# Performance work log

Measured on AMD Instinct MI355X. Metric: run time of the kernel, lower is better.

Reference implementation:

```python
import jax, jax.numpy as jnp
import numpy as np

N_HEAD = 16
DIMS = 1024

def setup_inputs() -> dict:
    key = jax.random.key(0)
    ks = jax.random.split(key, 5)
    B, T, C = 4, 2048, DIMS
    std = 1.0 / np.sqrt(C)
    x = jax.random.normal(ks[0], (B, T, C), dtype=jnp.float32)
    W_attn = jax.random.normal(ks[1], (C, 3 * C), dtype=jnp.float32) * std
    b_attn = jnp.zeros((3 * C,), dtype=jnp.float32)
    W_proj = jax.random.normal(ks[2], (C, C), dtype=jnp.float32) * std
    b_proj = jnp.zeros((C,), dtype=jnp.float32)
    return {"x": x, "W_attn": W_attn, "b_attn": b_attn, "W_proj": W_proj, "b_proj": b_proj}

def reference(x, W_attn, b_attn, W_proj, b_proj):
    B, T, C = x.shape
    H = N_HEAD
    D = C // H
    qkv = x @ W_attn + b_attn  # [B,T,3C]
    q, k, v = jnp.split(qkv, 3, axis=-1)
    # [B,T,C] -> [B,H,T,D]
    q = q.reshape(B, T, H, D).transpose(0, 2, 1, 3)
    k = k.reshape(B, T, H, D).transpose(0, 2, 1, 3)
    v = v.reshape(B, T, H, D).transpose(0, 2, 1, 3)
    att = jnp.einsum('bhqd,bhkd->bhqk', q, k) * (1.0 / np.sqrt(D))
    causal = jnp.tril(jnp.ones((T, T), dtype=bool))  # [T,T]
    att = jnp.where(causal[None, None, :, :], att, -jnp.inf)
    att = jax.nn.softmax(att, axis=-1)
    # dropout p=0.0 -> identity in eval/zero-prob mode
    y = jnp.einsum('bhqk,bhkd->bhqd', att, v)  # [B,H,T,D]
    y = y.transpose(0, 2, 1, 3).reshape(B, T, C)
    y = y @ W_proj + b_proj
    return y
```

## Files before the change

kernel.cpp:

```cpp
#include <hip/hip_runtime.h>
#include <hip/hip_bf16.h>
#include <stdint.h>

typedef unsigned short u16;
typedef unsigned int   u32;

using short8 = __attribute__((ext_vector_type(8))) short;
using f32x4  = __attribute__((ext_vector_type(4))) float;

__device__ __forceinline__ float b2f(u32 u) {
    union { u32 i; float f; } v;
    v.i = u << 16;
    return v.f;
}
__device__ __forceinline__ u16 f2b(float f) {
    union { float f; u32 i; } v; v.f = f;
    u32 x = v.i;
    x += 0x7fffu + ((x >> 16) & 1u);
    return (u16)(x >> 16);
}
__device__ __forceinline__ u32 pkbf16(float lo, float hi) {
    __hip_bfloat162 h = __float22bfloat162_rn(float2{lo, hi});
    return *reinterpret_cast<u32*>(&h);
}
__device__ __forceinline__ float fexp2(float x) {
#if __has_builtin(__builtin_amdgcn_exp2f)
    return __builtin_amdgcn_exp2f(x);
#else
    return exp2f(x);
#endif
}
__device__ __forceinline__ u32 perm_lo(u32 a, u32 b) {
#if __has_builtin(__builtin_amdgcn_perm)
    return __builtin_amdgcn_perm(b, a, 0x05040100u);
#else
    return (a & 0xffffu) | (b << 16);
#endif
}
__device__ __forceinline__ u32 perm_hi(u32 a, u32 b) {
#if __has_builtin(__builtin_amdgcn_perm)
    return __builtin_amdgcn_perm(b, a, 0x07060302u);
#else
    return (a >> 16) | (b & 0xffff0000u);
#endif
}

__device__ __forceinline__ void gll16(const u16* g, u16* l) {
    __builtin_amdgcn_global_load_lds(
        (const __attribute__((address_space(1))) void*)g,
        (__attribute__((address_space(3))) void*)l, 16, 0, 0);
}

__global__ __launch_bounds__(256)
void cast_bf16(const float* __restrict__ in, u16* __restrict__ out, int n)
{
    const int i = (blockIdx.x * 256 + threadIdx.x) * 8;
    if (i >= n) return;
    const float4 a = *reinterpret_cast<const float4*>(in + i);
    const float4 b = *reinterpret_cast<const float4*>(in + i + 4);
    *reinterpret_cast<uint4*>(out + i) = make_uint4(
        pkbf16(a.x, a.y), pkbf16(a.z, a.w), pkbf16(b.x, b.y), pkbf16(b.z, b.w));
}

__global__ __launch_bounds__(256)
void transpose_cast2(const float* __restrict__ Wa, u16* __restrict__ Wta,
                     const float* __restrict__ Wp, u16* __restrict__ Wtp)
{
    __shared__ float t[32][33];
    constexpr int R = 1024;
    const bool pa = blockIdx.x < 96;
    const float* W  = pa ? Wa  : Wp;
    u16*         Wt = pa ? Wta : Wtp;
    const int Ncols = pa ? 3072 : 1024;
    const int c0 = (pa ? blockIdx.x : blockIdx.x - 96) * 32;
    const int r0 = blockIdx.y * 32;
    const int lx = threadIdx.x & 31, ly = threadIdx.x >> 5;
#pragma unroll
    for (int i = 0; i < 4; i++) {
        const int r = ly + i * 8;
        t[r][lx] = W[(size_t)(r0 + r) * Ncols + c0 + lx];
    }
    __syncthreads();
#pragma unroll
    for (int i = 0; i < 4; i++) {
        const int c = ly + i * 8;
        Wt[(size_t)(c0 + c) * R + r0 + lx] = f2b(t[lx][c]);
    }
}

template<typename OT>
__global__ __launch_bounds__(256)
void gemm_mfma(const u16* __restrict__ A, const u16* __restrict__ Bt,
               const float* __restrict__ bias, OT* __restrict__ C,
               int M, int N, int K)
{
    __shared__ u16 As[128 * 32];
    __shared__ u16 Bs[128 * 32];

    const int tid  = threadIdx.x;
    const int w    = tid >> 6;
    const int lane = tid & 63;
    const int quad = lane >> 4;
    const int c16  = lane & 15;
    const int wr   = w >> 1, wc = w & 1;

    const int m0 = blockIdx.y * 128;
    const int n0 = blockIdx.x * 128;

    const int srow = w * 32 + (lane >> 2);
    const int skc  = (lane & 3) * 8;
    const u16* gA = A  + (size_t)(m0 + srow) * K + skc;
    const u16* gB = Bt + (size_t)(n0 + srow) * K + skc;
    u16* lA = As + w * 32 * 32 + lane * 8;
    u16* lB = Bs + w * 32 * 32 + lane * 8;

    f32x4 acc[4][4];
#pragma unroll
    for (int i = 0; i < 4; i++)
#pragma unroll
        for (int j = 0; j < 4; j++) acc[i][j] = (f32x4){0.f, 0.f, 0.f, 0.f};

    for (int k0 = 0; k0 < K; k0 += 32) {
        __syncthreads();
        gll16(gA + k0,                  lA);
        gll16(gA + k0 + 16 * (size_t)K, lA + 16 * 32);
        gll16(gB + k0,                  lB);
        gll16(gB + k0 + 16 * (size_t)K, lB + 16 * 32);
        __syncthreads();

        short8 af[4], bf[4];
#pragma unroll
        for (int i = 0; i < 4; i++)
            af[i] = *reinterpret_cast<const short8*>(&As[(wr * 64 + i * 16 + c16) * 32 + quad * 8]);
#pragma unroll
        for (int j = 0; j < 4; j++)
            bf[j] = *reinterpret_cast<const short8*>(&Bs[(wc * 64 + j * 16 + c16) * 32 + quad * 8]);
#pragma unroll
        for (int i = 0; i < 4; i++)
#pragma unroll
            for (int j = 0; j < 4; j++)
                acc[i][j] = __builtin_amdgcn_mfma_f32_16x16x32_bf16(af[i], bf[j], acc[i][j], 0, 0, 0);
    }

#pragma unroll
    for (int i = 0; i < 4; i++)
#pragma unroll
        for (int j = 0; j < 4; j++) {
            const int colg = n0 + wc * 64 + j * 16 + c16;
            const float bv = bias[colg];
#pragma unroll
            for (int r = 0; r < 4; r++) {
                const int rowg = m0 + wr * 64 + i * 16 + quad * 4 + r;
                const float v = acc[i][j][r] + bv;
                if constexpr (sizeof(OT) == 2)
                    ((u16*)C)[(size_t)rowg * N + colg] = f2b(v);
                else
                    ((float*)C)[(size_t)rowg * N + colg] = v;
            }
        }
}

__global__ __launch_bounds__(512, 2)
void gemm_mfma_256(const u16* __restrict__ A, const u16* __restrict__ Bt,
                   const float* __restrict__ bias, u16* __restrict__ C,
                   int M, int N, int K)
{
    __shared__ u16 ring[4 * 16384];

    const int tid  = threadIdx.x;
    const int w    = tid >> 6;
    const int lane = tid & 63;
    const int quad = lane >> 4;
    const int c16  = lane & 15;
    const int wr   = w >> 2;
    const int wc   = w & 3;

    const int nwg  = gridDim.x * gridDim.y;
    const int orig = blockIdx.y * gridDim.x + blockIdx.x;
    const int swz  = (orig & 7) * (nwg >> 3) + (orig >> 3);
    const int bx   = swz % gridDim.x;
    const int by   = swz / gridDim.x;
    const int m0   = by * 256, n0 = bx * 256;

    const int r0s = w * 16 + (lane >> 2);
    const int qs  = (lane & 3) ^ ((r0s >> 1) & 3);
    const u16* gA = A  + (size_t)(m0 + r0s) * K + qs * 8;
    const u16* gB = Bt + (size_t)(n0 + r0s) * K + qs * 8;
    const size_t hstep = (size_t)128 * K;
    u16* dstB = ring + w * 512 + lane * 8;

    const int slot = quad ^ ((c16 >> 1) & 3);
    const int aoff = (wr * 128 + c16) * 32 + slot * 8;
    const int boff = 8192 + (wc * 64 + c16) * 32 + slot * 8;

    f32x4 acc[8][4];
#pragma unroll
    for (int i = 0; i < 8; i++)
#pragma unroll
        for (int j = 0; j < 4; j++) acc[i][j] = (f32x4){0.f, 0.f, 0.f, 0.f};

    const int nt = K >> 5;

#pragma unroll
    for (int t = 0; t < 3; t++) {
        u16* db = dstB + t * 16384;
        const size_t ko = (size_t)t * 32;
        gll16(gA + ko,         db);
        gll16(gA + ko + hstep, db + 4096);
        gll16(gB + ko,         db + 8192);
        gll16(gB + ko + hstep, db + 12288);
    }

#pragma unroll 1
    for (int t = 0; t < nt; t++) {
        const int remain = nt - 1 - t;
        if (remain >= 2)      asm volatile("s_waitcnt vmcnt(8)" ::: "memory");
        else if (remain == 1) asm volatile("s_waitcnt vmcnt(4)" ::: "memory");
        else                  asm volatile("s_waitcnt vmcnt(0)" ::: "memory");
        asm volatile("s_barrier" ::: "memory");

        const u16* buf = ring + (t & 3) * 16384;
        const bool pf  = (t + 3) < nt;
        u16* db = dstB + ((t + 3) & 3) * 16384;
        const size_t ko = (size_t)(t + 3) * 32;

        short8 bfr[4], afr[4];

#pragma unroll
        for (int j = 0; j < 4; j++)
            bfr[j] = *reinterpret_cast<const short8*>(buf + boff + j * 512);
#pragma unroll
        for (int i = 0; i < 4; i++)
            afr[i] = *reinterpret_cast<const short8*>(buf + aoff + i * 512);
        if (pf) { gll16(gA + ko, db); gll16(gA + ko + hstep, db + 4096); }
        asm volatile("s_waitcnt lgkmcnt(0)" ::: "memory");
        __builtin_amdgcn_sched_barrier(0);
        __builtin_amdgcn_s_setprio(1);
#pragma unroll
        for (int i = 0; i < 4; i++)
#pragma unroll
            for (int j = 0; j < 4; j++)
                acc[i][j] = __builtin_amdgcn_mfma_f32_16x16x32_bf16(afr[i], bfr[j], acc[i][j], 0, 0, 0);
        __builtin_amdgcn_s_setprio(0);
        asm volatile("s_barrier" ::: "memory");

#pragma unroll
        for (int i = 0; i < 4; i++)
            afr[i] = *reinterpret_cast<const short8*>(buf + aoff + (i + 4) * 512);
        if (pf) { gll16(gB + ko, db + 8192); gll16(gB + ko + hstep, db + 12288); }
        asm volatile("s_waitcnt lgkmcnt(0)" ::: "memory");
        __builtin_amdgcn_sched_barrier(0);
        __builtin_amdgcn_s_setprio(1);
#pragma unroll
        for (int i = 0; i < 4; i++)
#pragma unroll
            for (int j = 0; j < 4; j++)
                acc[i + 4][j] = __builtin_amdgcn_mfma_f32_16x16x32_bf16(afr[i], bfr[j], acc[i + 4][j], 0, 0, 0);
        __builtin_amdgcn_s_setprio(0);
        asm volatile("s_barrier" ::: "memory");
    }

    float bv[4];
#pragma unroll
    for (int j = 0; j < 4; j++) bv[j] = bias[n0 + wc * 64 + j * 16 + c16];

    const int erow = wr * 16 + quad * 4;
    const int ecol = wc * 64 + c16;
#pragma unroll
    for (int i = 0; i < 8; i++) {
#pragma unroll
        for (int j = 0; j < 4; j++)
#pragma unroll
            for (int r = 0; r < 4; r++)
                ring[(erow + r) * 264 + ecol + j * 16] = f2b(acc[i][j][r] + bv[j]);
        __syncthreads();
#pragma unroll
        for (int rr = 0; rr < 2; rr++) {
            const int lr = rr * 16 + (tid >> 5);
            const int cc = (tid & 31) * 8;
            const uint4 vvec = *reinterpret_cast<const uint4*>(&ring[lr * 264 + cc]);
            const int gr = m0 + (lr >> 4) * 128 + i * 16 + (lr & 15);
            *reinterpret_cast<uint4*>(&C[(size_t)gr * N + n0 + cc]) = vvec;
        }
        __syncthreads();
    }
}

struct TileState {
    f32x4 O[4];
    float m, l;
    short8 qf[2];
    int qglob;
};

__device__ __forceinline__ void tile_pass(
    const u16* __restrict__ Ks, const u16* __restrict__ Vt,
    u16* __restrict__ plrow,
    TileState& ts, int kt0, bool diag, int quad, int c16)
{
    const int x7 = c16 & 7;

    f32x4 s[4];
    __builtin_amdgcn_s_setprio(1);
#pragma unroll
    for (int sub = 0; sub < 4; sub++) {
        const int row = sub * 16 + c16;
        short8 kf0 = *reinterpret_cast<const short8*>(&Ks[row * 64 + ((0 + quad) ^ x7) * 8]);
        short8 kf1 = *reinterpret_cast<const short8*>(&Ks[row * 64 + ((4 + quad) ^ x7) * 8]);
        f32x4 acc = (f32x4){0.f, 0.f, 0.f, 0.f};
        acc = __builtin_amdgcn_mfma_f32_16x16x32_bf16(kf0, ts.qf[0], acc, 0, 0, 0);
        acc = __builtin_amdgcn_mfma_f32_16x16x32_bf16(kf1, ts.qf[1], acc, 0, 0, 0);
        s[sub] = acc;
    }
    __builtin_amdgcn_s_setprio(0);

    if (diag) {
#pragma unroll
        for (int sub = 0; sub < 4; sub++)
#pragma unroll
            for (int r = 0; r < 4; r++)
                if (kt0 + sub * 16 + quad * 4 + r > ts.qglob) s[sub][r] = -INFINITY;
    }

    float m0a = fmaxf(fmaxf(s[0][0], s[0][1]), fmaxf(s[0][2], s[0][3]));
    float m1a = fmaxf(fmaxf(s[1][0], s[1][1]), fmaxf(s[1][2], s[1][3]));
    float m2a = fmaxf(fmaxf(s[2][0], s[2][1]), fmaxf(s[2][2], s[2][3]));
    float m3a = fmaxf(fmaxf(s[3][0], s[3][1]), fmaxf(s[3][2], s[3][3]));
    float mloc = fmaxf(fmaxf(m0a, m1a), fmaxf(m2a, m3a));
    mloc = fmaxf(mloc, __shfl_xor(mloc, 16));
    mloc = fmaxf(mloc, __shfl_xor(mloc, 32));

    if (!__all(mloc <= ts.m + 8.f)) {
        const float mnew = fmaxf(ts.m, mloc);
        const float al   = fexp2(ts.m - mnew);
        ts.m = mnew;
        ts.l *= al;
#pragma unroll
        for (int r = 0; r < 4; r++) {
            const float alr = __shfl(al, quad * 4 + r);
#pragma unroll
            for (int d = 0; d < 4; d++) ts.O[d][r] *= alr;
        }
    }

    float ls = 0.f;
#pragma unroll
    for (int sub = 0; sub < 4; sub++) {
#pragma unroll
        for (int r = 0; r < 4; r++) s[sub][r] = fexp2(s[sub][r] - ts.m);
        ls += (s[sub][0] + s[sub][1]) + (s[sub][2] + s[sub][3]);
        *reinterpret_cast<uint2*>(
            plrow + c16 * 64 + ((sub * 2 + (quad >> 1)) ^ x7) * 8 + (quad & 1) * 4) =
            make_uint2(pkbf16(s[sub][0], s[sub][1]), pkbf16(s[sub][2], s[sub][3]));
    }
    ts.l += ls;

    short8 pf[2];
#pragma unroll
    for (int c = 0; c < 2; c++)
        pf[c] = *reinterpret_cast<const short8*>(
            plrow + c16 * 64 + ((c * 4 + quad) ^ x7) * 8);

    __builtin_amdgcn_s_setprio(1);
#pragma unroll
    for (int dsub = 0; dsub < 4; dsub++) {
        const int row = dsub * 16 + c16;
#pragma unroll
        for (int c = 0; c < 2; c++) {
            short8 vf = *reinterpret_cast<const short8*>(&Vt[row * 64 + ((c * 4 + quad) ^ x7) * 8]);
            ts.O[dsub] = __builtin_amdgcn_mfma_f32_16x16x32_bf16(pf[c], vf, ts.O[dsub], 0, 0, 0);
        }
    }
    __builtin_amdgcn_s_setprio(0);
}

__global__ __launch_bounds__(256)
void attn_flash(const u16* __restrict__ qkv, u16* __restrict__ out)
{
    constexpr int T = 2048, C = 1024, C3 = 3072;

    __shared__ u16 Ks[2][64 * 64];
    __shared__ u16 Vt[2][64 * 64];
    __shared__ u16 Pl[4][16 * 64];

    const int tid  = threadIdx.x;
    const int w    = tid >> 6;
    const int lane = tid & 63;
    const int quad = lane >> 4;
    const int c16  = lane & 15;

    const int flat = blockIdx.y * gridDim.x + blockIdx.x;
    const int xcd  = flat & 7;
    const int tt   = flat >> 3;
    const int qp   = tt & 15;
    const int bh   = ((tt >> 4) << 3) | xcd;
    const int qtA  = qp;
    const int qtB  = 31 - qp;
    const int h    = bh & 15;
    const int b    = bh >> 4;

    const int kr  = tid >> 2, kq = tid & 3;
    const int vkp = tid & 31, vdg = (tid >> 5) * 8;
    const u16* baseK = qkv + (size_t)(b * T + kr) * C3 + C + h * 64 + kq * 16;
    const u16* baseV = qkv + (size_t)(b * T + 2 * vkp) * C3 + 2 * C + h * 64 + vdg;

    const int kx  = kr & 7;
    const int kd0 = kr * 64 + ((2 * kq + 0) ^ kx) * 8;
    const int kd1 = kr * 64 + ((2 * kq + 1) ^ kx) * 8;
    const int vslot = vkp >> 2, vintra = (vkp & 3) * 2;

    u16* plrow = &Pl[w][0];

    uint4 ka, kb, va, vb;

#pragma unroll 1
    for (int phase = 0; phase < 2; ++phase) {
        const int qt = phase ? qtA : qtB;

        TileState ts;
        ts.qglob = qt * 64 + w * 16 + c16;
        ts.m = -INFINITY;
        ts.l = 0.f;
#pragma unroll
        for (int d = 0; d < 4; d++) ts.O[d] = (f32x4){0.f, 0.f, 0.f, 0.f};
        constexpr float QSCALE = 0.125f * 1.44269504089f;
#pragma unroll
        for (int c = 0; c < 2; c++) {
            short8 rq = *reinterpret_cast<const short8*>(
                qkv + (size_t)(b * T + ts.qglob) * C3 + h * 64 + c * 32 + quad * 8);
#pragma unroll
            for (int j = 0; j < 8; j++)
                ts.qf[c][j] = (short)f2b(b2f((u16)rq[j]) * QSCALE);
        }

        {
            const uint4* gp = reinterpret_cast<const uint4*>(baseK);
            ka = gp[0]; kb = gp[1];
            va = *reinterpret_cast<const uint4*>(baseV);
            vb = *reinterpret_cast<const uint4*>(baseV + C3);
        }
        __syncthreads();
        {
            *reinterpret_cast<uint4*>(&Ks[0][kd0]) = ka;
            *reinterpret_cast<uint4*>(&Ks[0][kd1]) = kb;
            const u32* aw = reinterpret_cast<const u32*>(&va);
            const u32* bw = reinterpret_cast<const u32*>(&vb);
#pragma unroll
            for (int i = 0; i < 4; i++) {
                const int d0 = vdg + 2 * i;
                *reinterpret_cast<u32*>(&Vt[0][d0 * 64 + (vslot ^ (2 * i)) * 8 + vintra]) =
                    perm_lo(aw[i], bw[i]);
                *reinterpret_cast<u32*>(&Vt[0][(d0 + 1) * 64 + (vslot ^ (2 * i + 1)) * 8 + vintra]) =
                    perm_hi(aw[i], bw[i]);
            }
        }

        for (int kt = 0; kt <= qt; kt++) {
            const int cur = kt & 1;
            __syncthreads();

            if (kt < qt) {
                const int nk0 = (kt + 1) * 64;
                const uint4* gp = reinterpret_cast<const uint4*>(baseK + (size_t)nk0 * C3);
                ka = gp[0]; kb = gp[1];
                const u16* g0 = baseV + (size_t)nk0 * C3;
                va = *reinterpret_cast<const uint4*>(g0);
                vb = *reinterpret_cast<const uint4*>(g0 + C3);
            }

            tile_pass(Ks[cur], Vt[cur], plrow, ts, kt * 64, kt == qt, quad, c16);

            if (kt < qt) {
                const int nxt = cur ^ 1;
                *reinterpret_cast<uint4*>(&Ks[nxt][kd0]) = ka;
                *reinterpret_cast<uint4*>(&Ks[nxt][kd1]) = kb;
                const u32* aw = reinterpret_cast<const u32*>(&va);
                const u32* bw = reinterpret_cast<const u32*>(&vb);
#pragma unroll
                for (int i = 0; i < 4; i++) {
                    const int d0 = vdg + 2 * i;
                    *reinterpret_cast<u32*>(&Vt[nxt][d0 * 64 + (vslot ^ (2 * i)) * 8 + vintra]) =
                        perm_lo(aw[i], bw[i]);
                    *reinterpret_cast<u32*>(&Vt[nxt][(d0 + 1) * 64 + (vslot ^ (2 * i + 1)) * 8 + vintra]) =
                        perm_hi(aw[i], bw[i]);
                }
            }
        }

        float ls = ts.l;
        ls += __shfl_xor(ls, 16);
        ls += __shfl_xor(ls, 32);
        const float inv = 1.0f / ls;
#pragma unroll
        for (int r = 0; r < 4; r++) {
            const float invr = __shfl(inv, quad * 4 + r);
            const int qrow = qt * 64 + w * 16 + quad * 4 + r;
#pragma unroll
            for (int dsub = 0; dsub < 4; dsub++)
                out[(size_t)(b * T + qrow) * C + h * 64 + dsub * 16 + c16] =
                    f2b(ts.O[dsub][r] * invr);
        }
    }
}

extern "C" void kernel_launch(void* const* d_in, const int* in_sizes, int n_in,
                              void* d_out, int out_size, void* d_ws, size_t ws_size,
                              hipStream_t stream)
{
    constexpr int B = 4, T = 2048, C = 1024;
    constexpr int M = B * T;
    const float* x      = (const float*)d_in[0];
    const float* W_attn = (const float*)d_in[1];
    const float* b_attn = (const float*)d_in[2];
    const float* W_proj = (const float*)d_in[3];
    const float* b_proj = (const float*)d_in[4];
    float* out = (float*)d_out;

    char* p = (char*)d_ws;
    u16* qkv     = (u16*)p;                 p += (size_t)M * 3 * C * sizeof(u16);
    u16* xb      = (u16*)p;
    u16* attn_o  = (u16*)p;                 p += (size_t)M * C * sizeof(u16);
    u16* Wt_attn = (u16*)p;                 p += (size_t)3 * C * C * sizeof(u16);
    u16* Wt_proj = (u16*)p;

    cast_bf16<<<dim3(M * C / (256 * 8)), 256, 0, stream>>>(x, xb, M * C);
    transpose_cast2<<<dim3(128, 32), 256, 0, stream>>>(W_attn, Wt_attn, W_proj, Wt_proj);

    gemm_mfma_256<<<dim3(3 * C / 256, M / 256), 512, 0, stream>>>(
        xb, Wt_attn, b_attn, qkv, M, 3 * C, C);

    attn_flash<<<dim3(16, B * 16), 256, 0, stream>>>(qkv, attn_o);

    gemm_mfma<float><<<dim3(C / 128, M / 128), 256, 0, stream>>>(
        attn_o, Wt_proj, b_proj, out, M, C, C);
}
```

Baseline: 270.4 us.

## Process 128-row query tiles per block with two 16-row groups per wave

Each wave now handles 32 query rows as two independent 16-row groups that share every K and V fragment loaded from LDS, so the block covers a 128-row query tile. The grid is halved to 8x64 blocks, each still pairing a low and a high query tile for causal load balance. The aim is to halve the number of K/V tile loads per query row and raise the ratio of MFMA work to LDS traffic. The cost is doubled accumulator and softmax state per wave, with higher register pressure, fewer blocks in flight, and some wasted work on partially masked diagonal tiles.

```diff
diff --git a/kernel.cpp b/kernel.cpp
--- a/kernel.cpp
+++ b/kernel.cpp
@@ -286,80 +286,88 @@
     }
 }
 
-struct TileState {
-    f32x4 O[4];
-    float m, l;
-    short8 qf[2];
-    int qglob;
+struct TileState2 {
+    f32x4 O[2][4];
+    float m[2], l[2];
+    short8 qf[2][2];
+    int qbase;
 };
 
-__device__ __forceinline__ void tile_pass(
+__device__ __forceinline__ void tile_pass2(
     const u16* __restrict__ Ks, const u16* __restrict__ Vt,
     u16* __restrict__ plrow,
-    TileState& ts, int kt0, bool diag, int quad, int c16)
+    TileState2& ts, int kt0, int quad, int c16)
 {
     const int x7 = c16 & 7;
 
-    f32x4 s[4];
+    f32x4 s[2][4];
     __builtin_amdgcn_s_setprio(1);
 #pragma unroll
     for (int sub = 0; sub < 4; sub++) {
         const int row = sub * 16 + c16;
         short8 kf0 = *reinterpret_cast<const short8*>(&Ks[row * 64 + ((0 + quad) ^ x7) * 8]);
         short8 kf1 = *reinterpret_cast<const short8*>(&Ks[row * 64 + ((4 + quad) ^ x7) * 8]);
-        f32x4 acc = (f32x4){0.f, 0.f, 0.f, 0.f};
-        acc = __builtin_amdgcn_mfma_f32_16x16x32_bf16(kf0, ts.qf[0], acc, 0, 0, 0);
-        acc = __builtin_amdgcn_mfma_f32_16x16x32_bf16(kf1, ts.qf[1], acc, 0, 0, 0);
-        s[sub] = acc;
+        f32x4 a0 = (f32x4){0.f, 0.f, 0.f, 0.f};
+        a0 = __builtin_amdgcn_mfma_f32_16x16x32_bf16(kf0, ts.qf[0][0], a0, 0, 0, 0);
+        s[0][sub] = __builtin_amdgcn_mfma_f32_16x16x32_bf16(kf1, ts.qf[0][1], a0, 0, 0, 0);
+        f32x4 a1 = (f32x4){0.f, 0.f, 0.f, 0.f};
+        a1 = __builtin_amdgcn_mfma_f32_16x16x32_bf16(kf0, ts.qf[1][0], a1, 0, 0, 0);
+        s[1][sub] = __builtin_amdgcn_mfma_f32_16x16x32_bf16(kf1, ts.qf[1][1], a1, 0, 0, 0);
     }
     __builtin_amdgcn_s_setprio(0);
 
-    if (diag) {
-#pragma unroll
-        for (int sub = 0; sub < 4; sub++)
-#pragma unroll
-            for (int r = 0; r < 4; r++)
-                if (kt0 + sub * 16 + quad * 4 + r > ts.qglob) s[sub][r] = -INFINITY;
-    }
-
-    float m0a = fmaxf(fmaxf(s[0][0], s[0][1]), fmaxf(s[0][2], s[0][3]));
-    float m1a = fmaxf(fmaxf(s[1][0], s[1][1]), fmaxf(s[1][2], s[1][3]));
-    float m2a = fmaxf(fmaxf(s[2][0], s[2][1]), fmaxf(s[2][2], s[2][3]));
-    float m3a = fmaxf(fmaxf(s[3][0], s[3][1]), fmaxf(s[3][2], s[3][3]));
-    float mloc = fmaxf(fmaxf(m0a, m1a), fmaxf(m2a, m3a));
-    mloc = fmaxf(mloc, __shfl_xor(mloc, 16));
-    mloc = fmaxf(mloc, __shfl_xor(mloc, 32));
-
-    if (!__all(mloc <= ts.m + 8.f)) {
-        const float mnew = fmaxf(ts.m, mloc);
-        const float al   = fexp2(ts.m - mnew);
-        ts.m = mnew;
-        ts.l *= al;
-#pragma unroll
-        for (int r = 0; r < 4; r++) {
-            const float alr = __shfl(al, quad * 4 + r);
-#pragma unroll
-            for (int d = 0; d < 4; d++) ts.O[d][r] *= alr;
-        }
-    }
-
-    float ls = 0.f;
-#pragma unroll
-    for (int sub = 0; sub < 4; sub++) {
-#pragma unroll
-        for (int r = 0; r < 4; r++) s[sub][r] = fexp2(s[sub][r] - ts.m);
-        ls += (s[sub][0] + s[sub][1]) + (s[sub][2] + s[sub][3]);
-        *reinterpret_cast<uint2*>(
-            plrow + c16 * 64 + ((sub * 2 + (quad >> 1)) ^ x7) * 8 + (quad & 1) * 4) =
-            make_uint2(pkbf16(s[sub][0], s[sub][1]), pkbf16(s[sub][2], s[sub][3]));
-    }
-    ts.l += ls;
-
-    short8 pf[2];
-#pragma unroll
-    for (int c = 0; c < 2; c++)
-        pf[c] = *reinterpret_cast<const short8*>(
-            plrow + c16 * 64 + ((c * 4 + quad) ^ x7) * 8);
+#pragma unroll
+    for (int g = 0; g < 2; g++) {
+        const int qg = ts.qbase + g * 16 + c16;
+        if (kt0 + 63 > ts.qbase + g * 16) {
+#pragma unroll
+            for (int sub = 0; sub < 4; sub++)
+#pragma unroll
+                for (int r = 0; r < 4; r++)
+                    if (kt0 + sub * 16 + quad * 4 + r > qg) s[g][sub][r] = -INFINITY;
+        }
+
+        float m0a = fmaxf(fmaxf(s[g][0][0], s[g][0][1]), fmaxf(s[g][0][2], s[g][0][3]));
+        float m1a = fmaxf(fmaxf(s[g][1][0], s[g][1][1]), fmaxf(s[g][1][2], s[g][1][3]));
+        float m2a = fmaxf(fmaxf(s[g][2][0], s[g][2][1]), fmaxf(s[g][2][2], s[g][2][3]));
+        float m3a = fmaxf(fmaxf(s[g][3][0], s[g][3][1]), fmaxf(s[g][3][2], s[g][3][3]));
+        float mloc = fmaxf(fmaxf(m0a, m1a), fmaxf(m2a, m3a));
+        mloc = fmaxf(mloc, __shfl_xor(mloc, 16));
+        mloc = fmaxf(mloc, __shfl_xor(mloc, 32));
+
+        if (!__all(mloc <= ts.m[g] + 8.f)) {
+            const float mnew = fmaxf(ts.m[g], mloc);
+            const float al   = fexp2(ts.m[g] - mnew);
+            ts.m[g] = mnew;
+            ts.l[g] *= al;
+#pragma unroll
+            for (int r = 0; r < 4; r++) {
+                const float alr = __shfl(al, quad * 4 + r);
+#pragma unroll
+                for (int d = 0; d < 4; d++) ts.O[g][d][r] *= alr;
+            }
+        }
+
+        float ls = 0.f;
+#pragma unroll
+        for (int sub = 0; sub < 4; sub++) {
+#pragma unroll
+            for (int r = 0; r < 4; r++) s[g][sub][r] = fexp2(s[g][sub][r] - ts.m[g]);
+            ls += (s[g][sub][0] + s[g][sub][1]) + (s[g][sub][2] + s[g][sub][3]);
+            *reinterpret_cast<uint2*>(
+                plrow + (g * 16 + c16) * 64 + ((sub * 2 + (quad >> 1)) ^ x7) * 8 + (quad & 1) * 4) =
+                make_uint2(pkbf16(s[g][sub][0], s[g][sub][1]), pkbf16(s[g][sub][2], s[g][sub][3]));
+        }
+        ts.l[g] += ls;
+    }
+
+    short8 pf[2][2];
+#pragma unroll
+    for (int g = 0; g < 2; g++)
+#pragma unroll
+        for (int c = 0; c < 2; c++)
+            pf[g][c] = *reinterpret_cast<const short8*>(
+                plrow + (g * 16 + c16) * 64 + ((c * 4 + quad) ^ x7) * 8);
 
     __builtin_amdgcn_s_setprio(1);
 #pragma unroll
@@ -368,7 +376,8 @@
 #pragma unroll
         for (int c = 0; c < 2; c++) {
             short8 vf = *reinterpret_cast<const short8*>(&Vt[row * 64 + ((c * 4 + quad) ^ x7) * 8]);
-            ts.O[dsub] = __builtin_amdgcn_mfma_f32_16x16x32_bf16(pf[c], vf, ts.O[dsub], 0, 0, 0);
+            ts.O[0][dsub] = __builtin_amdgcn_mfma_f32_16x16x32_bf16(pf[0][c], vf, ts.O[0][dsub], 0, 0, 0);
+            ts.O[1][dsub] = __builtin_amdgcn_mfma_f32_16x16x32_bf16(pf[1][c], vf, ts.O[1][dsub], 0, 0, 0);
         }
     }
     __builtin_amdgcn_s_setprio(0);
@@ -381,7 +390,7 @@
 
     __shared__ u16 Ks[2][64 * 64];
     __shared__ u16 Vt[2][64 * 64];
-    __shared__ u16 Pl[4][16 * 64];
+    __shared__ u16 Pl[4][32 * 64];
 
     const int tid  = threadIdx.x;
     const int w    = tid >> 6;
@@ -392,10 +401,10 @@
     const int flat = blockIdx.y * gridDim.x + blockIdx.x;
     const int xcd  = flat & 7;
     const int tt   = flat >> 3;
-    const int qp   = tt & 15;
-    const int bh   = ((tt >> 4) << 3) | xcd;
+    const int qp   = tt & 7;
+    const int bh   = ((tt >> 3) << 3) | xcd;
     const int qtA  = qp;
-    const int qtB  = 31 - qp;
+    const int qtB  = 15 - qp;
     const int h    = bh & 15;
     const int b    = bh >> 4;
 
@@ -417,21 +426,28 @@
     for (int phase = 0; phase < 2; ++phase) {
         const int qt = phase ? qtA : qtB;
 
-        TileState ts;
-        ts.qglob = qt * 64 + w * 16 + c16;
-        ts.m = -INFINITY;
-        ts.l = 0.f;
-#pragma unroll
-        for (int d = 0; d < 4; d++) ts.O[d] = (f32x4){0.f, 0.f, 0.f, 0.f};
+        TileState2 ts;
+        ts.qbase = qt * 128 + w * 32;
+        ts.m[0] = ts.m[1] = -INFINITY;
+        ts.l[0] = ts.l[1] = 0.f;
+#pragma unroll
+        for (int g = 0; g < 2; g++)
+#pragma unroll
+            for (int d = 0; d < 4; d++) ts.O[g][d] = (f32x4){0.f, 0.f, 0.f, 0.f};
         constexpr float QSCALE = 0.125f * 1.44269504089f;
 #pragma unroll
-        for (int c = 0; c < 2; c++) {
-            short8 rq = *reinterpret_cast<const short8*>(
-                qkv + (size_t)(b * T + ts.qglob) * C3 + h * 64 + c * 32 + quad * 8);
-#pragma unroll
-            for (int j = 0; j < 8; j++)
-                ts.qf[c][j] = (short)f2b(b2f((u16)rq[j]) * QSCALE);
-        }
+        for (int g = 0; g < 2; g++)
+#pragma unroll
+            for (int c = 0; c < 2; c++) {
+                short8 rq = *reinterpret_cast<const short8*>(
+                    qkv + (size_t)(b * T + ts.qbase + g * 16 + c16) * C3 + h * 64 + c * 32 + quad * 8);
+#pragma unroll
+                for (int j = 0; j < 8; j++)
+                    ts.qf[g][c][j] = (short)f2b(b2f((u16)rq[j]) * QSCALE);
+            }
+
+        const int ktmax = 2 * qt + 1;
+        const int qwmax = ts.qbase + 31;
 
         {
             const uint4* gp = reinterpret_cast<const uint4*>(baseK);
@@ -455,11 +471,11 @@
             }
         }
 
-        for (int kt = 0; kt <= qt; kt++) {
+        for (int kt = 0; kt <= ktmax; kt++) {
             const int cur = kt & 1;
             __syncthreads();
 
-            if (kt < qt) {
+            if (kt < ktmax) {
                 const int nk0 = (kt + 1) * 64;
                 const uint4* gp = reinterpret_cast<const uint4*>(baseK + (size_t)nk0 * C3);
                 ka = gp[0]; kb = gp[1];
@@ -468,9 +484,10 @@
                 vb = *reinterpret_cast<const uint4*>(g0 + C3);
             }
 
-            tile_pass(Ks[cur], Vt[cur], plrow, ts, kt * 64, kt == qt, quad, c16);
-
-            if (kt < qt) {
+            if (kt * 64 <= qwmax)
+                tile_pass2(Ks[cur], Vt[cur], plrow, ts, kt * 64, quad, c16);
+
+            if (kt < ktmax) {
                 const int nxt = cur ^ 1;
                 *reinterpret_cast<uint4*>(&Ks[nxt][kd0]) = ka;
                 *reinterpret_cast<uint4*>(&Ks[nxt][kd1]) = kb;
@@ -487,18 +504,21 @@
             }
         }
 
-        float ls = ts.l;
-        ls += __shfl_xor(ls, 16);
-        ls += __shfl_xor(ls, 32);
-        const float inv = 1.0f / ls;
-#pragma unroll
-        for (int r = 0; r < 4; r++) {
-            const float invr = __shfl(inv, quad * 4 + r);
-            const int qrow = qt * 64 + w * 16 + quad * 4 + r;
-#pragma unroll
-            for (int dsub = 0; dsub < 4; dsub++)
-                out[(size_t)(b * T + qrow) * C + h * 64 + dsub * 16 + c16] =
-                    f2b(ts.O[dsub][r] * invr);
+#pragma unroll
+        for (int g = 0; g < 2; g++) {
+            float ls = ts.l[g];
+            ls += __shfl_xor(ls, 16);
+            ls += __shfl_xor(ls, 32);
+            const float inv = 1.0f / ls;
+#pragma unroll
+            for (int r = 0; r < 4; r++) {
+                const float invr = __shfl(inv, quad * 4 + r);
+                const int qrow = ts.qbase + g * 16 + quad * 4 + r;
+#pragma unroll
+                for (int dsub = 0; dsub < 4; dsub++)
+                    out[(size_t)(b * T + qrow) * C + h * 64 + dsub * 16 + c16] =
+                        f2b(ts.O[g][dsub][r] * invr);
+            }
         }
     }
 }
@@ -529,7 +549,7 @@
     gemm_mfma_256<<<dim3(3 * C / 256, M / 256), 512, 0, stream>>>(
         xb, Wt_attn, b_attn, qkv, M, 3 * C, C);
 
-    attn_flash<<<dim3(16, B * 16), 256, 0, stream>>>(qkv, attn_o);
+    attn_flash<<<dim3(8, B * 16), 256, 0, stream>>>(qkv, attn_o);
 
     gemm_mfma<float><<<dim3(C / 128, M / 128), 256, 0, stream>>>(
         attn_o, Wt_proj, b_proj, out, M, C, C);
```

After: 264.7 us. -2.1%, faster.

## Use 128-row query tiles with 8 waves in flash attention; fuse prep kernels

Applied to the files above, without the earlier changes.

The attention kernel now runs 512 threads (8 waves) per block, so each block covers 128 query rows per phase instead of 64 and every K/V tile loaded into LDS is shared by twice as many waves. K and V staging is split between two halves of the block, and waves skip key tiles beyond their causal range. The grid is halved and the causal pairing of query tiles is adjusted to match. The x cast and weight transpose-cast are merged into one prep launch to save a kernel launch. Larger blocks can reduce occupancy and leave some waves idle on the diagonal tiles.

```diff
diff --git a/kernel.cpp b/kernel.cpp
--- a/kernel.cpp
+++ b/kernel.cpp
@@ -52,28 +52,29 @@
 }
 
 __global__ __launch_bounds__(256)
-void cast_bf16(const float* __restrict__ in, u16* __restrict__ out, int n)
-{
-    const int i = (blockIdx.x * 256 + threadIdx.x) * 8;
-    if (i >= n) return;
-    const float4 a = *reinterpret_cast<const float4*>(in + i);
-    const float4 b = *reinterpret_cast<const float4*>(in + i + 4);
-    *reinterpret_cast<uint4*>(out + i) = make_uint4(
-        pkbf16(a.x, a.y), pkbf16(a.z, a.w), pkbf16(b.x, b.y), pkbf16(b.z, b.w));
-}
-
-__global__ __launch_bounds__(256)
-void transpose_cast2(const float* __restrict__ Wa, u16* __restrict__ Wta,
-                     const float* __restrict__ Wp, u16* __restrict__ Wtp)
+void prep(const float* __restrict__ x, u16* __restrict__ xb,
+          const float* __restrict__ Wa, u16* __restrict__ Wta,
+          const float* __restrict__ Wp, u16* __restrict__ Wtp)
 {
     __shared__ float t[32][33];
+    const int bx = blockIdx.x;
+    if (bx < 4096) {
+        const int i = (bx * 256 + threadIdx.x) * 8;
+        const float4 a = *reinterpret_cast<const float4*>(x + i);
+        const float4 b = *reinterpret_cast<const float4*>(x + i + 4);
+        *reinterpret_cast<uint4*>(xb + i) = make_uint4(
+            pkbf16(a.x, a.y), pkbf16(a.z, a.w), pkbf16(b.x, b.y), pkbf16(b.z, b.w));
+        return;
+    }
     constexpr int R = 1024;
-    const bool pa = blockIdx.x < 96;
+    const int tb = bx - 4096;
+    const int cb = tb & 127;
+    const int r0 = (tb >> 7) * 32;
+    const bool pa = cb < 96;
     const float* W  = pa ? Wa  : Wp;
     u16*         Wt = pa ? Wta : Wtp;
     const int Ncols = pa ? 3072 : 1024;
-    const int c0 = (pa ? blockIdx.x : blockIdx.x - 96) * 32;
-    const int r0 = blockIdx.y * 32;
+    const int c0 = (pa ? cb : cb - 96) * 32;
     const int lx = threadIdx.x & 31, ly = threadIdx.x >> 5;
 #pragma unroll
     for (int i = 0; i < 4; i++) {
@@ -286,17 +287,17 @@
     }
 }
 
-struct TileState {
+struct TileState1 {
     f32x4 O[4];
     float m, l;
     short8 qf[2];
-    int qglob;
+    int qbase;
 };
 
-__device__ __forceinline__ void tile_pass(
+__device__ __forceinline__ void tile_pass1(
     const u16* __restrict__ Ks, const u16* __restrict__ Vt,
     u16* __restrict__ plrow,
-    TileState& ts, int kt0, bool diag, int quad, int c16)
+    TileState1& ts, int kt0, int quad, int c16)
 {
     const int x7 = c16 & 7;
 
@@ -307,19 +308,19 @@
         const int row = sub * 16 + c16;
         short8 kf0 = *reinterpret_cast<const short8*>(&Ks[row * 64 + ((0 + quad) ^ x7) * 8]);
         short8 kf1 = *reinterpret_cast<const short8*>(&Ks[row * 64 + ((4 + quad) ^ x7) * 8]);
-        f32x4 acc = (f32x4){0.f, 0.f, 0.f, 0.f};
-        acc = __builtin_amdgcn_mfma_f32_16x16x32_bf16(kf0, ts.qf[0], acc, 0, 0, 0);
-        acc = __builtin_amdgcn_mfma_f32_16x16x32_bf16(kf1, ts.qf[1], acc, 0, 0, 0);
-        s[sub] = acc;
+        f32x4 a = (f32x4){0.f, 0.f, 0.f, 0.f};
+        a = __builtin_amdgcn_mfma_f32_16x16x32_bf16(kf0, ts.qf[0], a, 0, 0, 0);
+        s[sub] = __builtin_amdgcn_mfma_f32_16x16x32_bf16(kf1, ts.qf[1], a, 0, 0, 0);
     }
     __builtin_amdgcn_s_setprio(0);
 
-    if (diag) {
+    if (kt0 + 63 > ts.qbase) {
+        const int qg = ts.qbase + c16;
 #pragma unroll
         for (int sub = 0; sub < 4; sub++)
 #pragma unroll
             for (int r = 0; r < 4; r++)
-                if (kt0 + sub * 16 + quad * 4 + r > ts.qglob) s[sub][r] = -INFINITY;
+                if (kt0 + sub * 16 + quad * 4 + r > qg) s[sub][r] = -INFINITY;
     }
 
     float m0a = fmaxf(fmaxf(s[0][0], s[0][1]), fmaxf(s[0][2], s[0][3]));
@@ -374,14 +375,14 @@
     __builtin_amdgcn_s_setprio(0);
 }
 
-__global__ __launch_bounds__(256)
+__global__ __launch_bounds__(512)
 void attn_flash(const u16* __restrict__ qkv, u16* __restrict__ out)
 {
     constexpr int T = 2048, C = 1024, C3 = 3072;
 
     __shared__ u16 Ks[2][64 * 64];
     __shared__ u16 Vt[2][64 * 64];
-    __shared__ u16 Pl[4][16 * 64];
+    __shared__ u16 Pl[8][16 * 64];
 
     const int tid  = threadIdx.x;
     const int w    = tid >> 6;
@@ -392,15 +393,17 @@
     const int flat = blockIdx.y * gridDim.x + blockIdx.x;
     const int xcd  = flat & 7;
     const int tt   = flat >> 3;
-    const int qp   = tt & 15;
-    const int bh   = ((tt >> 4) << 3) | xcd;
+    const int qp   = tt & 7;
+    const int bh   = ((tt >> 3) << 3) | xcd;
     const int qtA  = qp;
-    const int qtB  = 31 - qp;
+    const int qtB  = 15 - qp;
     const int h    = bh & 15;
     const int b    = bh >> 4;
 
-    const int kr  = tid >> 2, kq = tid & 3;
-    const int vkp = tid & 31, vdg = (tid >> 5) * 8;
+    const bool stK = tid < 256;
+    const int st   = stK ? tid : tid - 256;
+    const int kr  = st >> 2, kq = st & 3;
+    const int vkp = st & 31, vdg = (st >> 5) * 8;
     const u16* baseK = qkv + (size_t)(b * T + kr) * C3 + C + h * 64 + kq * 16;
     const u16* baseV = qkv + (size_t)(b * T + 2 * vkp) * C3 + 2 * C + h * 64 + vdg;
 
@@ -411,14 +414,14 @@
 
     u16* plrow = &Pl[w][0];
 
-    uint4 ka, kb, va, vb;
+    uint4 ra, rb;
 
 #pragma unroll 1
     for (int phase = 0; phase < 2; ++phase) {
         const int qt = phase ? qtA : qtB;
 
-        TileState ts;
-        ts.qglob = qt * 64 + w * 16 + c16;
+        TileState1 ts;
+        ts.qbase = qt * 128 + w * 16;
         ts.m = -INFINITY;
         ts.l = 0.f;
 #pragma unroll
@@ -427,24 +430,29 @@
 #pragma unroll
         for (int c = 0; c < 2; c++) {
             short8 rq = *reinterpret_cast<const short8*>(
-                qkv + (size_t)(b * T + ts.qglob) * C3 + h * 64 + c * 32 + quad * 8);
+                qkv + (size_t)(b * T + ts.qbase + c16) * C3 + h * 64 + c * 32 + quad * 8);
 #pragma unroll
             for (int j = 0; j < 8; j++)
                 ts.qf[c][j] = (short)f2b(b2f((u16)rq[j]) * QSCALE);
         }
 
-        {
+        const int ktmax = 2 * qt + 1;
+        const int qwmax = ts.qbase + 15;
+
+        if (stK) {
             const uint4* gp = reinterpret_cast<const uint4*>(baseK);
-            ka = gp[0]; kb = gp[1];
-            va = *reinterpret_cast<const uint4*>(baseV);
-            vb = *reinterpret_cast<const uint4*>(baseV + C3);
+            ra = gp[0]; rb = gp[1];
+        } else {
+            ra = *reinterpret_cast<const uint4*>(baseV);
+            rb = *reinterpret_cast<const uint4*>(baseV + C3);
         }
         __syncthreads();
-        {
-            *reinterpret_cast<uint4*>(&Ks[0][kd0]) = ka;
-            *reinterpret_cast<uint4*>(&Ks[0][kd1]) = kb;
-            const u32* aw = reinterpret_cast<const u32*>(&va);
-            const u32* bw = reinterpret_cast<const u32*>(&vb);
+        if (stK) {
+            *reinterpret_cast<uint4*>(&Ks[0][kd0]) = ra;
+            *reinterpret_cast<uint4*>(&Ks[0][kd1]) = rb;
+        } else {
+            const u32* aw = reinterpret_cast<const u32*>(&ra);
+            const u32* bw = reinterpret_cast<const u32*>(&rb);
 #pragma unroll
             for (int i = 0; i < 4; i++) {
                 const int d0 = vdg + 2 * i;
@@ -455,50 +463,59 @@
             }
         }
 
-        for (int kt = 0; kt <= qt; kt++) {
+        for (int kt = 0; kt <= ktmax; kt++) {
             const int cur = kt & 1;
             __syncthreads();
 
-            if (kt < qt) {
-                const int nk0 = (kt + 1) * 64;
-                const uint4* gp = reinterpret_cast<const uint4*>(baseK + (size_t)nk0 * C3);
-                ka = gp[0]; kb = gp[1];
-                const u16* g0 = baseV + (size_t)nk0 * C3;
-                va = *reinterpret_cast<const uint4*>(g0);
-                vb = *reinterpret_cast<const uint4*>(g0 + C3);
-            }
-
-            tile_pass(Ks[cur], Vt[cur], plrow, ts, kt * 64, kt == qt, quad, c16);
-
-            if (kt < qt) {
-                const int nxt = cur ^ 1;
-                *reinterpret_cast<uint4*>(&Ks[nxt][kd0]) = ka;
-                *reinterpret_cast<uint4*>(&Ks[nxt][kd1]) = kb;
-                const u32* aw = reinterpret_cast<const u32*>(&va);
-                const u32* bw = reinterpret_cast<const u32*>(&vb);
-#pragma unroll
-                for (int i = 0; i < 4; i++) {
-                    const int d0 = vdg + 2 * i;
-                    *reinterpret_cast<u32*>(&Vt[nxt][d0 * 64 + (vslot ^ (2 * i)) * 8 + vintra]) =
-                        perm_lo(aw[i], bw[i]);
-                    *reinterpret_cast<u32*>(&Vt[nxt][(d0 + 1) * 64 + (vslot ^ (2 * i + 1)) * 8 + vintra]) =
-                        perm_hi(aw[i], bw[i]);
+            if (kt < ktmax) {
+                const size_t nk0 = (size_t)(kt + 1) * 64;
+                if (stK) {
+                    const uint4* gp = reinterpret_cast<const uint4*>(baseK + nk0 * C3);
+                    ra = gp[0]; rb = gp[1];
+                } else {
+                    const u16* g0 = baseV + nk0 * C3;
+                    ra = *reinterpret_cast<const uint4*>(g0);
+                    rb = *reinterpret_cast<const uint4*>(g0 + C3);
                 }
             }
-        }
-
-        float ls = ts.l;
-        ls += __shfl_xor(ls, 16);
-        ls += __shfl_xor(ls, 32);
-        const float inv = 1.0f / ls;
-#pragma unroll
-        for (int r = 0; r < 4; r++) {
-            const float invr = __shfl(inv, quad * 4 + r);
-            const int qrow = qt * 64 + w * 16 + quad * 4 + r;
-#pragma unroll
-            for (int dsub = 0; dsub < 4; dsub++)
-                out[(size_t)(b * T + qrow) * C + h * 64 + dsub * 16 + c16] =
-                    f2b(ts.O[dsub][r] * invr);
+
+            if (kt * 64 <= qwmax)
+                tile_pass1(Ks[cur], Vt[cur], plrow, ts, kt * 64, quad, c16);
+
+            if (kt < ktmax) {
+                const int nxt = cur ^ 1;
+                if (stK) {
+                    *reinterpret_cast<uint4*>(&Ks[nxt][kd0]) = ra;
+                    *reinterpret_cast<uint4*>(&Ks[nxt][kd1]) = rb;
+                } else {
+                    const u32* aw = reinterpret_cast<const u32*>(&ra);
+                    const u32* bw = reinterpret_cast<const u32*>(&rb);
+#pragma unroll
+                    for (int i = 0; i < 4; i++) {
+                        const int d0 = vdg + 2 * i;
+                        *reinterpret_cast<u32*>(&Vt[nxt][d0 * 64 + (vslot ^ (2 * i)) * 8 + vintra]) =
+                            perm_lo(aw[i], bw[i]);
+                        *reinterpret_cast<u32*>(&Vt[nxt][(d0 + 1) * 64 + (vslot ^ (2 * i + 1)) * 8 + vintra]) =
+                            perm_hi(aw[i], bw[i]);
+                    }
+                }
+            }
+        }
+
+        {
+            float lsv = ts.l;
+            lsv += __shfl_xor(lsv, 16);
+            lsv += __shfl_xor(lsv, 32);
+            const float inv = 1.0f / lsv;
+#pragma unroll
+            for (int r = 0; r < 4; r++) {
+                const float invr = __shfl(inv, quad * 4 + r);
+                const int qrow = ts.qbase + quad * 4 + r;
+#pragma unroll
+                for (int dsub = 0; dsub < 4; dsub++)
+                    out[(size_t)(b * T + qrow) * C + h * 64 + dsub * 16 + c16] =
+                        f2b(ts.O[dsub][r] * invr);
+            }
         }
     }
 }
@@ -523,13 +540,12 @@
     u16* Wt_attn = (u16*)p;                 p += (size_t)3 * C * C * sizeof(u16);
     u16* Wt_proj = (u16*)p;
 
-    cast_bf16<<<dim3(M * C / (256 * 8)), 256, 0, stream>>>(x, xb, M * C);
-    transpose_cast2<<<dim3(128, 32), 256, 0, stream>>>(W_attn, Wt_attn, W_proj, Wt_proj);
+    prep<<<dim3(8192), 256, 0, stream>>>(x, xb, W_attn, Wt_attn, W_proj, Wt_proj);
 
     gemm_mfma_256<<<dim3(3 * C / 256, M / 256), 512, 0, stream>>>(
         xb, Wt_attn, b_attn, qkv, M, 3 * C, C);
 
-    attn_flash<<<dim3(16, B * 16), 256, 0, stream>>>(qkv, attn_o);
+    attn_flash<<<dim3(8, B * 16), 512, 0, stream>>>(qkv, attn_o);
 
     gemm_mfma<float><<<dim3(C / 128, M / 128), 256, 0, stream>>>(
         attn_o, Wt_proj, b_proj, out, M, C, C);
```

New measurement: 287.3 us. 1.06x slower.
